# Performance work log

Hardware: AMD Instinct MI355X
Metric: run time of the kernel (lower is better)

Reference implementation:

```python
import jax, jax.numpy as jnp
import numpy as np

D3D, D2D, DTEXT, DPROJ, SEQ_LEN = 256, 768, 3072, 3072, 256
B, S, T = 32, 256, 512


def setup_inputs() -> dict:
    key = jax.random.key(0)
    ks = jax.random.split(key, 9)
    s3 = 1.0 / np.sqrt(D3D)
    s2 = 1.0 / np.sqrt(D2D)
    sf = 1.0 / np.sqrt(DPROJ * 3)
    return {
        "feat_3d": jax.random.normal(ks[0], (B, D3D), jnp.float32),
        "feat_2d": jax.random.normal(ks[1], (B, S, D2D), jnp.float32),
        "feat_text": jax.random.normal(ks[2], (B, T, DTEXT), jnp.float32),
        "W3d": jax.random.uniform(ks[3], (DPROJ, D3D), jnp.float32, -s3, s3),
        "b3d": jax.random.uniform(ks[4], (DPROJ,), jnp.float32, -s3, s3),
        "W2d": jax.random.uniform(ks[5], (DPROJ, D2D), jnp.float32, -s2, s2),
        "b2d": jax.random.uniform(ks[6], (DPROJ,), jnp.float32, -s2, s2),
        "Wf": jax.random.uniform(ks[7], (DPROJ, DPROJ * 3), jnp.float32, -sf, sf),
        "bf": jax.random.uniform(ks[8], (DPROJ,), jnp.float32, -sf, sf),
    }


def reference(feat_3d, feat_2d, feat_text, W3d, b3d, W2d, b2d, Wf, bf):
    # Projections
    f3p = feat_3d @ W3d.T + b3d                      # [B, P]
    f2p = jnp.einsum("bsd,pd->bsp", feat_2d, W2d) + b2d  # [B, S, P]

    # Attention pooling of 2D slice features against global 3D feature
    scores_s = jnp.einsum("bsp,bp->bs", f2p, f3p)    # [B, S]
    w_s = jax.nn.softmax(scores_s, axis=1)
    pooled_2d = jnp.einsum("bs,bsp->bp", w_s, f2p)   # [B, P]

    # Attention pooling of text features against global 3D feature
    scores_t = jnp.einsum("btp,bp->bt", feat_text, f3p)  # [B, T]
    w_t = jax.nn.softmax(scores_t, axis=1)
    pooled_text = jnp.einsum("bt,btp->bp", w_t, feat_text)  # [B, P]

    # All seq_len rows of the original's concatenated input are identical,
    # so compute the fusion GEMM once per batch element and broadcast.
    fused_vec = jnp.concatenate([f3p, pooled_2d, pooled_text], axis=-1) @ Wf.T + bf  # [B, P]
    return jnp.broadcast_to(fused_vec[:, None, :], (fused_vec.shape[0], SEQ_LEN, fused_vec.shape[1]))
```

## Files before the change

### kernel.cpp

```cpp
#include <hip/hip_runtime.h>

#define NB 32
#define NS 256
#define NT 512
#define KD3 256
#define KD2 768
#define NP 3072
#define KFZ 9216

__global__ __launch_bounds__(256) void k1_f3p(const float* __restrict__ f3d,
                                              const float* __restrict__ W3d,
                                              const float* __restrict__ b3d,
                                              float* __restrict__ concatb) {
  int b = blockIdx.x & 31, pc = blockIdx.x >> 5;
  __shared__ float4 xs[KD3 / 4];
  int tid = threadIdx.x;
  if (tid < KD3 / 4) xs[tid] = ((const float4*)(f3d + b * KD3))[tid];
  __syncthreads();
  int p = pc * 256 + tid;
  const float4* wrow = (const float4*)(W3d + (size_t)p * KD3);
  float acc = b3d[p];
#pragma unroll 8
  for (int i = 0; i < KD3 / 4; ++i) {
    float4 w = wrow[i], x = xs[i];
    acc = fmaf(w.x, x.x, acc); acc = fmaf(w.y, x.y, acc);
    acc = fmaf(w.z, x.z, acc); acc = fmaf(w.w, x.w, acc);
  }
  concatb[(size_t)b * KFZ + p] = acc;
}

__global__ __launch_bounds__(256) void k2_gpart(const float* __restrict__ W2d,
                                                const float* __restrict__ concatb,
                                                float* __restrict__ g_part) {
  int dc = blockIdx.x % 3, kc = blockIdx.x / 3;
  __shared__ float xs[NB * 96];
  int tid = threadIdx.x;
  int p0 = kc * 96;
  for (int i = tid; i < NB * 96; i += 256) {
    int bb = i / 96, pp = i - bb * 96;
    xs[i] = concatb[(size_t)bb * KFZ + p0 + pp];
  }
  __syncthreads();
  int d = dc * 256 + tid;
  float acc[NB];
#pragma unroll
  for (int b = 0; b < NB; ++b) acc[b] = 0.f;
  for (int pp = 0; pp < 96; pp += 4) {
    float w0 = W2d[(size_t)(p0 + pp + 0) * KD2 + d];
    float w1 = W2d[(size_t)(p0 + pp + 1) * KD2 + d];
    float w2 = W2d[(size_t)(p0 + pp + 2) * KD2 + d];
    float w3 = W2d[(size_t)(p0 + pp + 3) * KD2 + d];
#pragma unroll
    for (int b = 0; b < NB; ++b) {
      float4 x4 = *(const float4*)&xs[b * 96 + pp];
      acc[b] = fmaf(w0, x4.x, acc[b]); acc[b] = fmaf(w1, x4.y, acc[b]);
      acc[b] = fmaf(w2, x4.z, acc[b]); acc[b] = fmaf(w3, x4.w, acc[b]);
    }
  }
#pragma unroll
  for (int b = 0; b < NB; ++b) g_part[(size_t)(kc * NB + b) * KD2 + d] = acc[b];
}

__global__ __launch_bounds__(256) void k3a_scores(const float* __restrict__ f2d,
                                                  const float* __restrict__ g_part,
                                                  float* __restrict__ w_s) {
  int b = blockIdx.x & 31, sc = blockIdx.x >> 5;
  __shared__ float g[KD2];
  int tid = threadIdx.x;
  for (int i = tid; i < KD2; i += 256) {
    float a = 0.f;
    for (int c = 0; c < 32; ++c) a += g_part[(size_t)(c * NB + b) * KD2 + i];
    g[i] = a;
  }
  __syncthreads();
  int wave = tid >> 6, lane = tid & 63;
  for (int i = 0; i < 16; ++i) {
    int s = sc * 64 + wave * 16 + i;
    const float4* row = (const float4*)(f2d + ((size_t)b * NS + s) * KD2);
    float acc = 0.f;
#pragma unroll
    for (int j = 0; j < 3; ++j) {
      float4 v = row[lane + 64 * j];
      float4 gg = *(const float4*)&g[4 * (lane + 64 * j)];
      acc = fmaf(v.x, gg.x, acc); acc = fmaf(v.y, gg.y, acc);
      acc = fmaf(v.z, gg.z, acc); acc = fmaf(v.w, gg.w, acc);
    }
#pragma unroll
    for (int o = 32; o; o >>= 1) acc += __shfl_xor(acc, o, 64);
    if (lane == 0) w_s[b * NS + s] = acc;
  }
}

template <int N>
__global__ __launch_bounds__(N) void k_softmax(float* __restrict__ w) {
  int b = blockIdx.x, tid = threadIdx.x;
  __shared__ float sm[N / 64];
  __shared__ float stat[2];
  float v = w[(size_t)b * N + tid];
  int wave = tid >> 6, lane = tid & 63;
  float m = v;
#pragma unroll
  for (int o = 32; o; o >>= 1) m = fmaxf(m, __shfl_xor(m, o, 64));
  if (lane == 0) sm[wave] = m;
  __syncthreads();
  if (tid == 0) {
    float mm = sm[0];
    for (int i = 1; i < N / 64; ++i) mm = fmaxf(mm, sm[i]);
    stat[0] = mm;
  }
  __syncthreads();
  float e = __expf(v - stat[0]);
  float s = e;
#pragma unroll
  for (int o = 32; o; o >>= 1) s += __shfl_xor(s, o, 64);
  __syncthreads();
  if (lane == 0) sm[wave] = s;
  __syncthreads();
  if (tid == 0) {
    float ss = 0.f;
    for (int i = 0; i < N / 64; ++i) ss += sm[i];
    stat[1] = ss;
  }
  __syncthreads();
  w[(size_t)b * N + tid] = e / stat[1];
}

__global__ __launch_bounds__(256) void k3c_pool2f(const float* __restrict__ f2d,
                                                  const float* __restrict__ w_s,
                                                  float* __restrict__ p2f) {
  int b = blockIdx.x / 3, dc = blockIdx.x % 3;
  __shared__ float w[NS];
  int tid = threadIdx.x;
  w[tid] = w_s[b * NS + tid];
  __syncthreads();
  int d = dc * 256 + tid;
  float acc = 0.f;
  for (int s = 0; s < NS; ++s)
    acc = fmaf(w[s], f2d[((size_t)b * NS + s) * KD2 + d], acc);
  p2f[b * KD2 + d] = acc;
}

__global__ __launch_bounds__(256) void k4a_scorest(const float* __restrict__ ftx,
                                                   const float* __restrict__ concatb,
                                                   float* __restrict__ w_t) {
  int b = blockIdx.x & 31, tc = blockIdx.x >> 5;
  __shared__ float4 f3[NP / 4];
  int tid = threadIdx.x;
  for (int i = tid; i < NP / 4; i += 256)
    f3[i] = ((const float4*)(concatb + (size_t)b * KFZ))[i];
  __syncthreads();
  int wave = tid >> 6, lane = tid & 63;
  for (int i = 0; i < 16; ++i) {
    int t = tc * 64 + wave * 16 + i;
    const float4* row = (const float4*)(ftx + ((size_t)b * NT + t) * NP);
    float acc = 0.f;
#pragma unroll
    for (int j = 0; j < 12; ++j) {
      float4 v = row[lane + 64 * j];
      float4 gg = f3[lane + 64 * j];
      acc = fmaf(v.x, gg.x, acc); acc = fmaf(v.y, gg.y, acc);
      acc = fmaf(v.z, gg.z, acc); acc = fmaf(v.w, gg.w, acc);
    }
#pragma unroll
    for (int o = 32; o; o >>= 1) acc += __shfl_xor(acc, o, 64);
    if (lane == 0) w_t[b * NT + t] = acc;
  }
}

__global__ __launch_bounds__(256) void k4c_poolt(const float* __restrict__ ftx,
                                                 const float* __restrict__ w_t,
                                                 float* __restrict__ ptp) {
  int b = blockIdx.x & 31;
  int r = blockIdx.x >> 5;
  int pc = r % 3, tc = r / 3;
  __shared__ float w[128];
  int tid = threadIdx.x;
  if (tid < 128) w[tid] = w_t[b * NT + tc * 128 + tid];
  __syncthreads();
  int p4 = pc * 1024 + 4 * tid;
  float4 acc = {0.f, 0.f, 0.f, 0.f};
  const float* base = ftx + ((size_t)b * NT + tc * 128) * NP + p4;
  for (int tt = 0; tt < 128; ++tt) {
    float4 v = *(const float4*)(base + (size_t)tt * NP);
    float ww = w[tt];
    acc.x = fmaf(ww, v.x, acc.x); acc.y = fmaf(ww, v.y, acc.y);
    acc.z = fmaf(ww, v.z, acc.z); acc.w = fmaf(ww, v.w, acc.w);
  }
  *(float4*)(ptp + (size_t)(tc * NB + b) * NP + p4) = acc;
}

__global__ __launch_bounds__(256) void k4d_red(const float* __restrict__ ptp,
                                               float* __restrict__ concatb) {
  int b = blockIdx.x & 31, pc = blockIdx.x >> 5;
  int p = pc * 256 + threadIdx.x;
  float a = 0.f;
#pragma unroll
  for (int c = 0; c < 4; ++c) a += ptp[(size_t)(c * NB + b) * NP + p];
  concatb[(size_t)b * KFZ + 2 * NP + p] = a;
}

__global__ __launch_bounds__(256) void k5_pool2d(const float* __restrict__ W2d,
                                                 const float* __restrict__ b2d,
                                                 const float* __restrict__ p2f,
                                                 float* __restrict__ concatb) {
  int bh = blockIdx.x & 1, pb = blockIdx.x >> 1;
  __shared__ float xs[16 * KD2];
  int tid = threadIdx.x;
  for (int i = tid; i < 16 * KD2; i += 256) xs[i] = p2f[(size_t)(bh * 16) * KD2 + i];
  __syncthreads();
  int wave = tid >> 6, lane = tid & 63;
  for (int pi = 0; pi < 4; ++pi) {
    int p = pb * 16 + wave * 4 + pi;
    const float4* row = (const float4*)(W2d + (size_t)p * KD2);
    float4 wv0 = row[lane], wv1 = row[lane + 64], wv2 = row[lane + 128];
    for (int bb = 0; bb < 16; ++bb) {
      const float* xb = &xs[bb * KD2];
      float4 x0 = *(const float4*)&xb[4 * lane];
      float4 x1 = *(const float4*)&xb[4 * (lane + 64)];
      float4 x2 = *(const float4*)&xb[4 * (lane + 128)];
      float acc = 0.f;
      acc = fmaf(wv0.x, x0.x, acc); acc = fmaf(wv0.y, x0.y, acc);
      acc = fmaf(wv0.z, x0.z, acc); acc = fmaf(wv0.w, x0.w, acc);
      acc = fmaf(wv1.x, x1.x, acc); acc = fmaf(wv1.y, x1.y, acc);
      acc = fmaf(wv1.z, x1.z, acc); acc = fmaf(wv1.w, x1.w, acc);
      acc = fmaf(wv2.x, x2.x, acc); acc = fmaf(wv2.y, x2.y, acc);
      acc = fmaf(wv2.z, x2.z, acc); acc = fmaf(wv2.w, x2.w, acc);
#pragma unroll
      for (int o = 32; o; o >>= 1) acc += __shfl_xor(acc, o, 64);
      if (lane == 0)
        concatb[(size_t)(bh * 16 + bb) * KFZ + NP + p] = acc + b2d[p];
    }
  }
}

__global__ __launch_bounds__(256) void k6_fused(const float* __restrict__ Wf,
                                                const float* __restrict__ concatb,
                                                float* __restrict__ fpart) {
  int kc = blockIdx.x & 15, pb = blockIdx.x >> 4;
  __shared__ float wt[128 * 68];
  __shared__ float xt[32 * 68];
  int tid = threadIdx.x;
  int tp = tid & 31, tb = tid >> 5;
  float acc[4][4];
#pragma unroll
  for (int i = 0; i < 4; ++i)
#pragma unroll
    for (int j = 0; j < 4; ++j) acc[i][j] = 0.f;
  int kbase = kc * 576;
  for (int kt = 0; kt < 9; ++kt) {
    int k0 = kbase + kt * 64;
#pragma unroll
    for (int it = 0; it < 8; ++it) {
      int i = tid + it * 256;
      int row = i >> 4, c4 = (i & 15) * 4;
      *(float4*)&wt[row * 68 + c4] =
          *(const float4*)&Wf[(size_t)(pb * 128 + row) * KFZ + k0 + c4];
    }
#pragma unroll
    for (int it = 0; it < 2; ++it) {
      int i = tid + it * 256;
      int row = i >> 4, c4 = (i & 15) * 4;
      *(float4*)&xt[row * 68 + c4] =
          *(const float4*)&concatb[(size_t)row * KFZ + k0 + c4];
    }
    __syncthreads();
#pragma unroll 4
    for (int kk = 0; kk < 64; kk += 4) {
      float4 wv[4], xv[4];
#pragma unroll
      for (int i = 0; i < 4; ++i) wv[i] = *(const float4*)&wt[(tp + 32 * i) * 68 + kk];
#pragma unroll
      for (int j = 0; j < 4; ++j) xv[j] = *(const float4*)&xt[(tb + 8 * j) * 68 + kk];
#pragma unroll
      for (int i = 0; i < 4; ++i)
#pragma unroll
        for (int j = 0; j < 4; ++j) {
          acc[i][j] = fmaf(wv[i].x, xv[j].x, acc[i][j]);
          acc[i][j] = fmaf(wv[i].y, xv[j].y, acc[i][j]);
          acc[i][j] = fmaf(wv[i].z, xv[j].z, acc[i][j]);
          acc[i][j] = fmaf(wv[i].w, xv[j].w, acc[i][j]);
        }
    }
    __syncthreads();
  }
#pragma unroll
  for (int i = 0; i < 4; ++i)
#pragma unroll
    for (int j = 0; j < 4; ++j)
      fpart[(size_t)(kc * NB + tb + 8 * j) * NP + pb * 128 + tp + 32 * i] = acc[i][j];
}

__global__ __launch_bounds__(256) void k7_bcast(const float* __restrict__ fpart,
                                                const float* __restrict__ bfv,
                                                float* __restrict__ out) {
  int b = blockIdx.x & 31;
  int r = blockIdx.x >> 5;
  int pc = r % 3, sc = r / 3;
  int tid = threadIdx.x;
  int p4 = pc * 1024 + 4 * tid;
  float4 v = *(const float4*)&bfv[p4];
#pragma unroll
  for (int c = 0; c < 16; ++c) {
    float4 a = *(const float4*)&fpart[(size_t)(c * NB + b) * NP + p4];
    v.x += a.x; v.y += a.y; v.z += a.z; v.w += a.w;
  }
  float* obase = out + (size_t)b * NS * NP + p4;
  for (int ss = 0; ss < 64; ++ss) {
    int s = sc * 64 + ss;
    *(float4*)(obase + (size_t)s * NP) = v;
  }
}

extern "C" void kernel_launch(void* const* d_in, const int* in_sizes, int n_in,
                              void* d_out, int out_size, void* d_ws, size_t ws_size,
                              hipStream_t stream) {
  const float* f3d = (const float*)d_in[0];
  const float* f2d = (const float*)d_in[1];
  const float* ftx = (const float*)d_in[2];
  const float* W3d = (const float*)d_in[3];
  const float* b3d = (const float*)d_in[4];
  const float* W2d = (const float*)d_in[5];
  const float* b2d = (const float*)d_in[6];
  const float* Wf  = (const float*)d_in[7];
  const float* bfv = (const float*)d_in[8];
  float* out = (float*)d_out;
  float* ws = (float*)d_ws;

  float* concatb = ws;
  float* g_part  = ws + 294912;
  float* w_s     = ws + 1081344;
  float* p2f     = ws + 1089536;
  float* w_t     = ws + 1114112;
  float* ptp     = ws + 1130496;
  float* fpart   = ws + 1523712;

  k1_f3p<<<384, 256, 0, stream>>>(f3d, W3d, b3d, concatb);
  k2_gpart<<<96, 256, 0, stream>>>(W2d, concatb, g_part);
  k3a_scores<<<128, 256, 0, stream>>>(f2d, g_part, w_s);
  k_softmax<256><<<32, 256, 0, stream>>>(w_s);
  k3c_pool2f<<<96, 256, 0, stream>>>(f2d, w_s, p2f);
  k4a_scorest<<<256, 256, 0, stream>>>(ftx, concatb, w_t);
  k_softmax<512><<<32, 512, 0, stream>>>(w_t);
  k4c_poolt<<<384, 256, 0, stream>>>(ftx, w_t, ptp);
  k4d_red<<<384, 256, 0, stream>>>(ptp, concatb);
  k5_pool2d<<<384, 256, 0, stream>>>(W2d, b2d, p2f, concatb);
  k6_fused<<<384, 256, 0, stream>>>(Wf, concatb, fpart);
  k7_bcast<<<384, 256, 0, stream>>>(fpart, bfv, out);
}
```

Before: 613.8 us.

## Restructure pipeline with online-softmax text pooling and merged multi-role kernels

Text scoring, softmax and pooling are fused into a single pass over feat_text using an online (flash-style) softmax. Per-chunk max/sum partials are merged in a later kernel, so the 200MB text tensor is read once instead of twice. Independent work (the W2d-based score GEMV and the text pass, then the 2D scores and the text reduction) is co-scheduled in the same launches, and the 2D softmax is folded into pooling. The pooled-2D projection becomes a split-K tiled GEMM writing to four partial concat buffers, and the fusion GEMM's tiles are enlarged. This cuts the kernel count from twelve to seven, at the cost of extra partial-buffer traffic and higher register pressure.

```diff
diff --git a/kernel.cpp b/kernel.cpp
--- a/kernel.cpp
+++ b/kernel.cpp
@@ -8,10 +8,22 @@
 #define NP 3072
 #define KFZ 9216
 
+__device__ __forceinline__ float wave_red_sum(float v) {
+#pragma unroll
+  for (int o = 32; o; o >>= 1) v += __shfl_xor(v, o, 64);
+  return v;
+}
+__device__ __forceinline__ float wave_red_max(float v) {
+#pragma unroll
+  for (int o = 32; o; o >>= 1) v = fmaxf(v, __shfl_xor(v, o, 64));
+  return v;
+}
+
 __global__ __launch_bounds__(256) void k1_f3p(const float* __restrict__ f3d,
                                               const float* __restrict__ W3d,
                                               const float* __restrict__ b3d,
-                                              float* __restrict__ concatb) {
+                                              float* __restrict__ c0, float* __restrict__ c1,
+                                              float* __restrict__ c2, float* __restrict__ c3) {
   int b = blockIdx.x & 31, pc = blockIdx.x >> 5;
   __shared__ float4 xs[KD3 / 4];
   int tid = threadIdx.x;
@@ -26,253 +38,226 @@
     acc = fmaf(w.x, x.x, acc); acc = fmaf(w.y, x.y, acc);
     acc = fmaf(w.z, x.z, acc); acc = fmaf(w.w, x.w, acc);
   }
-  concatb[(size_t)b * KFZ + p] = acc;
-}
-
-__global__ __launch_bounds__(256) void k2_gpart(const float* __restrict__ W2d,
-                                                const float* __restrict__ concatb,
-                                                float* __restrict__ g_part) {
-  int dc = blockIdx.x % 3, kc = blockIdx.x / 3;
-  __shared__ float xs[NB * 96];
-  int tid = threadIdx.x;
-  int p0 = kc * 96;
-  for (int i = tid; i < NB * 96; i += 256) {
-    int bb = i / 96, pp = i - bb * 96;
-    xs[i] = concatb[(size_t)bb * KFZ + p0 + pp];
-  }
+  size_t o = (size_t)b * KFZ + p;
+  c0[o] = acc; c1[o] = 0.f; c2[o] = 0.f; c3[o] = 0.f;
+}
+
+__global__ __launch_bounds__(256) void k_L2(const float* __restrict__ ftx,
+                                            const float* __restrict__ W2d,
+                                            const float* __restrict__ c0,
+                                            float* __restrict__ g_part,
+                                            float* __restrict__ Pt,
+                                            float* __restrict__ ml) {
+  __shared__ float4 smem4[768];
+  float* sm = (float*)smem4;
+  int tid = threadIdx.x;
+  if (blockIdx.x < 512) {
+    int b = blockIdx.x & 31, tch = blockIdx.x >> 5;
+    for (int i = tid; i < NP / 4; i += 256)
+      smem4[i] = ((const float4*)(c0 + (size_t)b * KFZ))[i];
+    __syncthreads();
+    int wave = tid >> 6, lane = tid & 63;
+    int t0 = tch * 32 + wave * 8;
+    float m = -3.0e38f, l = 0.f;
+    float4 acc[12];
+#pragma unroll
+    for (int j = 0; j < 12; ++j) acc[j] = make_float4(0.f, 0.f, 0.f, 0.f);
+    for (int r = 0; r < 8; ++r) {
+      const float4* row = (const float4*)(ftx + ((size_t)(b * NT + t0 + r)) * NP);
+      float4 xr[12];
+#pragma unroll
+      for (int j = 0; j < 12; ++j) xr[j] = row[lane + 64 * j];
+      float s = 0.f;
+#pragma unroll
+      for (int j = 0; j < 12; ++j) {
+        float4 f = smem4[lane + 64 * j];
+        s = fmaf(xr[j].x, f.x, s); s = fmaf(xr[j].y, f.y, s);
+        s = fmaf(xr[j].z, f.z, s); s = fmaf(xr[j].w, f.w, s);
+      }
+      s = wave_red_sum(s);
+      float mn = fmaxf(m, s);
+      float al = __expf(m - mn);
+      float e = __expf(s - mn);
+      l = fmaf(l, al, e);
+#pragma unroll
+      for (int j = 0; j < 12; ++j) {
+        acc[j].x = fmaf(acc[j].x, al, e * xr[j].x);
+        acc[j].y = fmaf(acc[j].y, al, e * xr[j].y);
+        acc[j].z = fmaf(acc[j].z, al, e * xr[j].z);
+        acc[j].w = fmaf(acc[j].w, al, e * xr[j].w);
+      }
+      m = mn;
+    }
+    int c = tch * 4 + wave;
+    float4* Pr = (float4*)(Pt + (size_t)(c * NB + b) * NP);
+#pragma unroll
+    for (int j = 0; j < 12; ++j) Pr[lane + 64 * j] = acc[j];
+    if (lane == 0) { ml[(c * NB + b) * 2] = m; ml[(c * NB + b) * 2 + 1] = l; }
+  } else {
+    int id = blockIdx.x - 512;
+    int dc = id % 3, kc = id / 3;
+    int p0 = kc * 96;
+    for (int i = tid; i < NB * 96; i += 256) {
+      int bb = i / 96, pp = i - bb * 96;
+      sm[i] = c0[(size_t)bb * KFZ + p0 + pp];
+    }
+    __syncthreads();
+    int d = dc * 256 + tid;
+    float acc[NB];
+#pragma unroll
+    for (int b = 0; b < NB; ++b) acc[b] = 0.f;
+    for (int pp = 0; pp < 96; pp += 4) {
+      float w0 = W2d[(size_t)(p0 + pp + 0) * KD2 + d];
+      float w1 = W2d[(size_t)(p0 + pp + 1) * KD2 + d];
+      float w2 = W2d[(size_t)(p0 + pp + 2) * KD2 + d];
+      float w3 = W2d[(size_t)(p0 + pp + 3) * KD2 + d];
+#pragma unroll
+      for (int b = 0; b < NB; ++b) {
+        float4 x4 = *(const float4*)&sm[b * 96 + pp];
+        acc[b] = fmaf(w0, x4.x, acc[b]); acc[b] = fmaf(w1, x4.y, acc[b]);
+        acc[b] = fmaf(w2, x4.z, acc[b]); acc[b] = fmaf(w3, x4.w, acc[b]);
+      }
+    }
+#pragma unroll
+    for (int b = 0; b < NB; ++b) g_part[(size_t)(kc * NB + b) * KD2 + d] = acc[b];
+  }
+}
+
+__global__ __launch_bounds__(256) void k_L3(const float* __restrict__ f2d,
+                                            const float* __restrict__ g_part,
+                                            float* __restrict__ sraw,
+                                            const float* __restrict__ Pt,
+                                            const float* __restrict__ ml,
+                                            float* __restrict__ c0, float* __restrict__ c1,
+                                            float* __restrict__ c2, float* __restrict__ c3) {
+  __shared__ float4 sh4[KD2 / 4];
+  float* sh = (float*)sh4;
+  int tid = threadIdx.x;
+  if (blockIdx.x < 128) {
+    int b = blockIdx.x & 31, sc = blockIdx.x >> 5;
+    for (int i = tid; i < KD2; i += 256) {
+      float a = 0.f;
+      for (int c = 0; c < 32; ++c) a += g_part[(size_t)(c * NB + b) * KD2 + i];
+      sh[i] = a;
+    }
+    __syncthreads();
+    int wave = tid >> 6, lane = tid & 63;
+    for (int i = 0; i < 16; ++i) {
+      int s = sc * 64 + wave * 16 + i;
+      const float4* row = (const float4*)(f2d + ((size_t)b * NS + s) * KD2);
+      float acc = 0.f;
+#pragma unroll
+      for (int j = 0; j < 3; ++j) {
+        float4 v = row[lane + 64 * j];
+        float4 g = sh4[lane + 64 * j];
+        acc = fmaf(v.x, g.x, acc); acc = fmaf(v.y, g.y, acc);
+        acc = fmaf(v.z, g.z, acc); acc = fmaf(v.w, g.w, acc);
+      }
+      acc = wave_red_sum(acc);
+      if (lane == 0) sraw[b * NS + s] = acc;
+    }
+  } else {
+    int id = blockIdx.x - 128;
+    int b = id & 31, pc = id >> 5;
+    if (tid < 64) {
+      sh[2 * tid] = ml[(tid * NB + b) * 2];
+      sh[2 * tid + 1] = ml[(tid * NB + b) * 2 + 1];
+    }
+    __syncthreads();
+    float M = -3.0e38f;
+    for (int c = 0; c < 64; ++c) M = fmaxf(M, sh[2 * c]);
+    float denom = 0.f;
+    for (int c = 0; c < 64; ++c) denom += __expf(sh[2 * c] - M) * sh[2 * c + 1];
+    float inv = 1.f / denom;
+    int p4 = pc * 1024 + tid * 4;
+    float4 a = make_float4(0.f, 0.f, 0.f, 0.f);
+    for (int c = 0; c < 64; ++c) {
+      float w = __expf(sh[2 * c] - M);
+      float4 v = *(const float4*)&Pt[(size_t)(c * NB + b) * NP + p4];
+      a.x = fmaf(w, v.x, a.x); a.y = fmaf(w, v.y, a.y);
+      a.z = fmaf(w, v.z, a.z); a.w = fmaf(w, v.w, a.w);
+    }
+    a.x *= inv; a.y *= inv; a.z *= inv; a.w *= inv;
+    size_t o = (size_t)b * KFZ + 2 * NP + p4;
+    float4 z = make_float4(0.f, 0.f, 0.f, 0.f);
+    *(float4*)&c0[o] = a;
+    *(float4*)&c1[o] = z; *(float4*)&c2[o] = z; *(float4*)&c3[o] = z;
+  }
+}
+
+__global__ __launch_bounds__(256) void k3c_sm(const float* __restrict__ f2d,
+                                              const float* __restrict__ sraw,
+                                              float* __restrict__ p2f) {
+  int b = blockIdx.x & 31;
+  int r = blockIdx.x >> 5;
+  int dc = r % 3, sc = r / 3;
+  __shared__ float pr[NS];
+  __shared__ float red[8];
+  int tid = threadIdx.x;
+  int wave = tid >> 6, lane = tid & 63;
+  float v = sraw[b * NS + tid];
+  float mx = wave_red_max(v);
+  if (lane == 0) red[wave] = mx;
   __syncthreads();
-  int d = dc * 256 + tid;
-  float acc[NB];
-#pragma unroll
-  for (int b = 0; b < NB; ++b) acc[b] = 0.f;
-  for (int pp = 0; pp < 96; pp += 4) {
-    float w0 = W2d[(size_t)(p0 + pp + 0) * KD2 + d];
-    float w1 = W2d[(size_t)(p0 + pp + 1) * KD2 + d];
-    float w2 = W2d[(size_t)(p0 + pp + 2) * KD2 + d];
-    float w3 = W2d[(size_t)(p0 + pp + 3) * KD2 + d];
-#pragma unroll
-    for (int b = 0; b < NB; ++b) {
-      float4 x4 = *(const float4*)&xs[b * 96 + pp];
-      acc[b] = fmaf(w0, x4.x, acc[b]); acc[b] = fmaf(w1, x4.y, acc[b]);
-      acc[b] = fmaf(w2, x4.z, acc[b]); acc[b] = fmaf(w3, x4.w, acc[b]);
-    }
-  }
-#pragma unroll
-  for (int b = 0; b < NB; ++b) g_part[(size_t)(kc * NB + b) * KD2 + d] = acc[b];
-}
-
-__global__ __launch_bounds__(256) void k3a_scores(const float* __restrict__ f2d,
-                                                  const float* __restrict__ g_part,
-                                                  float* __restrict__ w_s) {
-  int b = blockIdx.x & 31, sc = blockIdx.x >> 5;
-  __shared__ float g[KD2];
-  int tid = threadIdx.x;
-  for (int i = tid; i < KD2; i += 256) {
-    float a = 0.f;
-    for (int c = 0; c < 32; ++c) a += g_part[(size_t)(c * NB + b) * KD2 + i];
-    g[i] = a;
-  }
+  float M = fmaxf(fmaxf(red[0], red[1]), fmaxf(red[2], red[3]));
+  float e = __expf(v - M);
+  pr[tid] = e;
+  float smv = wave_red_sum(e);
+  if (lane == 0) red[4 + wave] = smv;
   __syncthreads();
-  int wave = tid >> 6, lane = tid & 63;
-  for (int i = 0; i < 16; ++i) {
-    int s = sc * 64 + wave * 16 + i;
-    const float4* row = (const float4*)(f2d + ((size_t)b * NS + s) * KD2);
-    float acc = 0.f;
-#pragma unroll
-    for (int j = 0; j < 3; ++j) {
-      float4 v = row[lane + 64 * j];
-      float4 gg = *(const float4*)&g[4 * (lane + 64 * j)];
-      acc = fmaf(v.x, gg.x, acc); acc = fmaf(v.y, gg.y, acc);
-      acc = fmaf(v.z, gg.z, acc); acc = fmaf(v.w, gg.w, acc);
-    }
-#pragma unroll
-    for (int o = 32; o; o >>= 1) acc += __shfl_xor(acc, o, 64);
-    if (lane == 0) w_s[b * NS + s] = acc;
-  }
-}
-
-template <int N>
-__global__ __launch_bounds__(N) void k_softmax(float* __restrict__ w) {
-  int b = blockIdx.x, tid = threadIdx.x;
-  __shared__ float sm[N / 64];
-  __shared__ float stat[2];
-  float v = w[(size_t)b * N + tid];
-  int wave = tid >> 6, lane = tid & 63;
-  float m = v;
-#pragma unroll
-  for (int o = 32; o; o >>= 1) m = fmaxf(m, __shfl_xor(m, o, 64));
-  if (lane == 0) sm[wave] = m;
-  __syncthreads();
-  if (tid == 0) {
-    float mm = sm[0];
-    for (int i = 1; i < N / 64; ++i) mm = fmaxf(mm, sm[i]);
-    stat[0] = mm;
-  }
-  __syncthreads();
-  float e = __expf(v - stat[0]);
-  float s = e;
-#pragma unroll
-  for (int o = 32; o; o >>= 1) s += __shfl_xor(s, o, 64);
-  __syncthreads();
-  if (lane == 0) sm[wave] = s;
-  __syncthreads();
-  if (tid == 0) {
-    float ss = 0.f;
-    for (int i = 0; i < N / 64; ++i) ss += sm[i];
-    stat[1] = ss;
-  }
-  __syncthreads();
-  w[(size_t)b * N + tid] = e / stat[1];
-}
-
-__global__ __launch_bounds__(256) void k3c_pool2f(const float* __restrict__ f2d,
-                                                  const float* __restrict__ w_s,
-                                                  float* __restrict__ p2f) {
-  int b = blockIdx.x / 3, dc = blockIdx.x % 3;
-  __shared__ float w[NS];
-  int tid = threadIdx.x;
-  w[tid] = w_s[b * NS + tid];
-  __syncthreads();
+  float inv = 1.f / (red[4] + red[5] + red[6] + red[7]);
   int d = dc * 256 + tid;
   float acc = 0.f;
-  for (int s = 0; s < NS; ++s)
-    acc = fmaf(w[s], f2d[((size_t)b * NS + s) * KD2 + d], acc);
-  p2f[b * KD2 + d] = acc;
-}
-
-__global__ __launch_bounds__(256) void k4a_scorest(const float* __restrict__ ftx,
-                                                   const float* __restrict__ concatb,
-                                                   float* __restrict__ w_t) {
-  int b = blockIdx.x & 31, tc = blockIdx.x >> 5;
-  __shared__ float4 f3[NP / 4];
-  int tid = threadIdx.x;
-  for (int i = tid; i < NP / 4; i += 256)
-    f3[i] = ((const float4*)(concatb + (size_t)b * KFZ))[i];
-  __syncthreads();
-  int wave = tid >> 6, lane = tid & 63;
-  for (int i = 0; i < 16; ++i) {
-    int t = tc * 64 + wave * 16 + i;
-    const float4* row = (const float4*)(ftx + ((size_t)b * NT + t) * NP);
-    float acc = 0.f;
-#pragma unroll
-    for (int j = 0; j < 12; ++j) {
-      float4 v = row[lane + 64 * j];
-      float4 gg = f3[lane + 64 * j];
-      acc = fmaf(v.x, gg.x, acc); acc = fmaf(v.y, gg.y, acc);
-      acc = fmaf(v.z, gg.z, acc); acc = fmaf(v.w, gg.w, acc);
-    }
-#pragma unroll
-    for (int o = 32; o; o >>= 1) acc += __shfl_xor(acc, o, 64);
-    if (lane == 0) w_t[b * NT + t] = acc;
-  }
-}
-
-__global__ __launch_bounds__(256) void k4c_poolt(const float* __restrict__ ftx,
-                                                 const float* __restrict__ w_t,
-                                                 float* __restrict__ ptp) {
-  int b = blockIdx.x & 31;
-  int r = blockIdx.x >> 5;
-  int pc = r % 3, tc = r / 3;
-  __shared__ float w[128];
-  int tid = threadIdx.x;
-  if (tid < 128) w[tid] = w_t[b * NT + tc * 128 + tid];
-  __syncthreads();
-  int p4 = pc * 1024 + 4 * tid;
-  float4 acc = {0.f, 0.f, 0.f, 0.f};
-  const float* base = ftx + ((size_t)b * NT + tc * 128) * NP + p4;
-  for (int tt = 0; tt < 128; ++tt) {
-    float4 v = *(const float4*)(base + (size_t)tt * NP);
-    float ww = w[tt];
-    acc.x = fmaf(ww, v.x, acc.x); acc.y = fmaf(ww, v.y, acc.y);
-    acc.z = fmaf(ww, v.z, acc.z); acc.w = fmaf(ww, v.w, acc.w);
-  }
-  *(float4*)(ptp + (size_t)(tc * NB + b) * NP + p4) = acc;
-}
-
-__global__ __launch_bounds__(256) void k4d_red(const float* __restrict__ ptp,
-                                               float* __restrict__ concatb) {
-  int b = blockIdx.x & 31, pc = blockIdx.x >> 5;
-  int p = pc * 256 + threadIdx.x;
-  float a = 0.f;
-#pragma unroll
-  for (int c = 0; c < 4; ++c) a += ptp[(size_t)(c * NB + b) * NP + p];
-  concatb[(size_t)b * KFZ + 2 * NP + p] = a;
+  const float* base = f2d + ((size_t)b * NS + sc * 128) * KD2 + d;
+#pragma unroll 8
+  for (int s = 0; s < 128; ++s)
+    acc = fmaf(pr[sc * 128 + s], base[(size_t)s * KD2], acc);
+  p2f[(size_t)(sc * NB + b) * KD2 + d] = acc * inv;
 }
 
 __global__ __launch_bounds__(256) void k5_pool2d(const float* __restrict__ W2d,
                                                  const float* __restrict__ b2d,
                                                  const float* __restrict__ p2f,
-                                                 float* __restrict__ concatb) {
-  int bh = blockIdx.x & 1, pb = blockIdx.x >> 1;
-  __shared__ float xs[16 * KD2];
-  int tid = threadIdx.x;
-  for (int i = tid; i < 16 * KD2; i += 256) xs[i] = p2f[(size_t)(bh * 16) * KD2 + i];
-  __syncthreads();
-  int wave = tid >> 6, lane = tid & 63;
-  for (int pi = 0; pi < 4; ++pi) {
-    int p = pb * 16 + wave * 4 + pi;
-    const float4* row = (const float4*)(W2d + (size_t)p * KD2);
-    float4 wv0 = row[lane], wv1 = row[lane + 64], wv2 = row[lane + 128];
-    for (int bb = 0; bb < 16; ++bb) {
-      const float* xb = &xs[bb * KD2];
-      float4 x0 = *(const float4*)&xb[4 * lane];
-      float4 x1 = *(const float4*)&xb[4 * (lane + 64)];
-      float4 x2 = *(const float4*)&xb[4 * (lane + 128)];
-      float acc = 0.f;
-      acc = fmaf(wv0.x, x0.x, acc); acc = fmaf(wv0.y, x0.y, acc);
-      acc = fmaf(wv0.z, x0.z, acc); acc = fmaf(wv0.w, x0.w, acc);
-      acc = fmaf(wv1.x, x1.x, acc); acc = fmaf(wv1.y, x1.y, acc);
-      acc = fmaf(wv1.z, x1.z, acc); acc = fmaf(wv1.w, x1.w, acc);
-      acc = fmaf(wv2.x, x2.x, acc); acc = fmaf(wv2.y, x2.y, acc);
-      acc = fmaf(wv2.z, x2.z, acc); acc = fmaf(wv2.w, x2.w, acc);
-#pragma unroll
-      for (int o = 32; o; o >>= 1) acc += __shfl_xor(acc, o, 64);
-      if (lane == 0)
-        concatb[(size_t)(bh * 16 + bb) * KFZ + NP + p] = acc + b2d[p];
-    }
-  }
-}
-
-__global__ __launch_bounds__(256) void k6_fused(const float* __restrict__ Wf,
-                                                const float* __restrict__ concatb,
-                                                float* __restrict__ fpart) {
-  int kc = blockIdx.x & 15, pb = blockIdx.x >> 4;
-  __shared__ float wt[128 * 68];
-  __shared__ float xt[32 * 68];
+                                                 float* __restrict__ c0, float* __restrict__ c1,
+                                                 float* __restrict__ c2, float* __restrict__ c3) {
+  int pb = blockIdx.x >> 2, ks = blockIdx.x & 3;
+  __shared__ __align__(16) float wt[64 * 68];
+  __shared__ __align__(16) float xt[32 * 68];
   int tid = threadIdx.x;
   int tp = tid & 31, tb = tid >> 5;
-  float acc[4][4];
-#pragma unroll
-  for (int i = 0; i < 4; ++i)
+  float acc[2][4];
+#pragma unroll
+  for (int i = 0; i < 2; ++i)
 #pragma unroll
     for (int j = 0; j < 4; ++j) acc[i][j] = 0.f;
-  int kbase = kc * 576;
-  for (int kt = 0; kt < 9; ++kt) {
-    int k0 = kbase + kt * 64;
-#pragma unroll
-    for (int it = 0; it < 8; ++it) {
-      int i = tid + it * 256;
-      int row = i >> 4, c4 = (i & 15) * 4;
+  for (int dk = 0; dk < 3; ++dk) {
+    int d0 = ks * 192 + dk * 64;
+#pragma unroll
+    for (int it = 0; it < 4; ++it) {
+      int idx = tid + it * 256;
+      int row = idx >> 4, c4 = (idx & 15) * 4;
       *(float4*)&wt[row * 68 + c4] =
-          *(const float4*)&Wf[(size_t)(pb * 128 + row) * KFZ + k0 + c4];
+          *(const float4*)&W2d[(size_t)(pb * 64 + row) * KD2 + d0 + c4];
     }
 #pragma unroll
     for (int it = 0; it < 2; ++it) {
-      int i = tid + it * 256;
-      int row = i >> 4, c4 = (i & 15) * 4;
-      *(float4*)&xt[row * 68 + c4] =
-          *(const float4*)&concatb[(size_t)row * KFZ + k0 + c4];
+      int idx = tid + it * 256;
+      int row = idx >> 4, c4 = (idx & 15) * 4;
+      float4 a = *(const float4*)&p2f[(size_t)row * KD2 + d0 + c4];
+      float4 bq = *(const float4*)&p2f[(size_t)(NB + row) * KD2 + d0 + c4];
+      a.x += bq.x; a.y += bq.y; a.z += bq.z; a.w += bq.w;
+      *(float4*)&xt[row * 68 + c4] = a;
     }
     __syncthreads();
 #pragma unroll 4
     for (int kk = 0; kk < 64; kk += 4) {
-      float4 wv[4], xv[4];
-#pragma unroll
-      for (int i = 0; i < 4; ++i) wv[i] = *(const float4*)&wt[(tp + 32 * i) * 68 + kk];
+      float4 wv[2], xv[4];
+#pragma unroll
+      for (int i = 0; i < 2; ++i) wv[i] = *(const float4*)&wt[(tp + 32 * i) * 68 + kk];
 #pragma unroll
       for (int j = 0; j < 4; ++j) xv[j] = *(const float4*)&xt[(tb + 8 * j) * 68 + kk];
 #pragma unroll
-      for (int i = 0; i < 4; ++i)
+      for (int i = 0; i < 2; ++i)
 #pragma unroll
         for (int j = 0; j < 4; ++j) {
           acc[i][j] = fmaf(wv[i].x, xv[j].x, acc[i][j]);
@@ -283,11 +268,80 @@
     }
     __syncthreads();
   }
-#pragma unroll
-  for (int i = 0; i < 4; ++i)
+  float* dst = (ks == 0) ? c0 : (ks == 1) ? c1 : (ks == 2) ? c2 : c3;
+#pragma unroll
+  for (int i = 0; i < 2; ++i) {
+    int p = pb * 64 + tp + 32 * i;
+    float bias = (ks == 0) ? b2d[p] : 0.f;
 #pragma unroll
     for (int j = 0; j < 4; ++j)
-      fpart[(size_t)(kc * NB + tb + 8 * j) * NP + pb * 128 + tp + 32 * i] = acc[i][j];
+      dst[(size_t)(tb + 8 * j) * KFZ + NP + p] = acc[i][j] + bias;
+  }
+}
+
+__global__ __launch_bounds__(256) void k6_fused(const float* __restrict__ Wf,
+                                                const float* __restrict__ c0,
+                                                const float* __restrict__ c1,
+                                                const float* __restrict__ c2,
+                                                const float* __restrict__ c3,
+                                                float* __restrict__ fpart) {
+  int pb = blockIdx.x >> 4, kc = blockIdx.x & 15;
+  __shared__ __align__(16) float wt[192 * 68];
+  __shared__ __align__(16) float xt[32 * 68];
+  int tid = threadIdx.x;
+  int tp = tid & 31, tb = tid >> 5;
+  float acc[6][4];
+#pragma unroll
+  for (int i = 0; i < 6; ++i)
+#pragma unroll
+    for (int j = 0; j < 4; ++j) acc[i][j] = 0.f;
+  for (int kt = 0; kt < 9; ++kt) {
+    int k0 = kc * 576 + kt * 64;
+#pragma unroll
+    for (int it = 0; it < 12; ++it) {
+      int idx = tid + it * 256;
+      int row = idx >> 4, c4 = (idx & 15) * 4;
+      *(float4*)&wt[row * 68 + c4] =
+          *(const float4*)&Wf[(size_t)(pb * 192 + row) * KFZ + k0 + c4];
+    }
+#pragma unroll
+    for (int it = 0; it < 2; ++it) {
+      int idx = tid + it * 256;
+      int row = idx >> 4, c4 = (idx & 15) * 4;
+      size_t o = (size_t)row * KFZ + k0 + c4;
+      float4 a = *(const float4*)&c0[o];
+      float4 v1 = *(const float4*)&c1[o];
+      float4 v2 = *(const float4*)&c2[o];
+      float4 v3 = *(const float4*)&c3[o];
+      a.x += v1.x + v2.x + v3.x; a.y += v1.y + v2.y + v3.y;
+      a.z += v1.z + v2.z + v3.z; a.w += v1.w + v2.w + v3.w;
+      *(float4*)&xt[row * 68 + c4] = a;
+    }
+    __syncthreads();
+#pragma unroll 4
+    for (int kk = 0; kk < 64; kk += 4) {
+      float4 wv[6], xv[4];
+#pragma unroll
+      for (int i = 0; i < 6; ++i) wv[i] = *(const float4*)&wt[(tp + 32 * i) * 68 + kk];
+#pragma unroll
+      for (int j = 0; j < 4; ++j) xv[j] = *(const float4*)&xt[(tb + 8 * j) * 68 + kk];
+#pragma unroll
+      for (int i = 0; i < 6; ++i)
+#pragma unroll
+        for (int j = 0; j < 4; ++j) {
+          acc[i][j] = fmaf(wv[i].x, xv[j].x, acc[i][j]);
+          acc[i][j] = fmaf(wv[i].y, xv[j].y, acc[i][j]);
+          acc[i][j] = fmaf(wv[i].z, xv[j].z, acc[i][j]);
+          acc[i][j] = fmaf(wv[i].w, xv[j].w, acc[i][j]);
+        }
+    }
+    __syncthreads();
+  }
+#pragma unroll
+  for (int i = 0; i < 6; ++i)
+#pragma unroll
+    for (int j = 0; j < 4; ++j)
+      fpart[(size_t)(kc * NB + tb + 8 * j) * NP + pb * 192 + tp + 32 * i] = acc[i][j];
 }
 
 __global__ __launch_bounds__(256) void k7_bcast(const float* __restrict__ fpart,
@@ -326,24 +380,22 @@
   float* out = (float*)d_out;
   float* ws = (float*)d_ws;
 
-  float* concatb = ws;
-  float* g_part  = ws + 294912;
-  float* w_s     = ws + 1081344;
-  float* p2f     = ws + 1089536;
-  float* w_t     = ws + 1114112;
-  float* ptp     = ws + 1130496;
-  float* fpart   = ws + 1523712;
-
-  k1_f3p<<<384, 256, 0, stream>>>(f3d, W3d, b3d, concatb);
-  k2_gpart<<<96, 256, 0, stream>>>(W2d, concatb, g_part);
-  k3a_scores<<<128, 256, 0, stream>>>(f2d, g_part, w_s);
-  k_softmax<256><<<32, 256, 0, stream>>>(w_s);
-  k3c_pool2f<<<96, 256, 0, stream>>>(f2d, w_s, p2f);
-  k4a_scorest<<<256, 256, 0, stream>>>(ftx, concatb, w_t);
-  k_softmax<512><<<32, 512, 0, stream>>>(w_t);
-  k4c_poolt<<<384, 256, 0, stream>>>(ftx, w_t, ptp);
-  k4d_red<<<384, 256, 0, stream>>>(ptp, concatb);
-  k5_pool2d<<<384, 256, 0, stream>>>(W2d, b2d, p2f, concatb);
-  k6_fused<<<384, 256, 0, stream>>>(Wf, concatb, fpart);
+  float* c0     = ws;
+  float* c1     = ws + 294912;
+  float* c2     = ws + 589824;
+  float* c3     = ws + 884736;
+  float* g_part = ws + 1179648;
+  float* sraw   = ws + 1966080;
+  float* p2f    = ws + 1974272;
+  float* ml     = ws + 2023424;
+  float* Pt     = ws + 2027520;
+  float* fpart  = ws + 8318976;
+
+  k1_f3p<<<384, 256, 0, stream>>>(f3d, W3d, b3d, c0, c1, c2, c3);
+  k_L2<<<608, 256, 0, stream>>>(ftx, W2d, c0, g_part, Pt, ml);
+  k_L3<<<224, 256, 0, stream>>>(f2d, g_part, sraw, Pt, ml, c0, c1, c2, c3);
+  k3c_sm<<<192, 256, 0, stream>>>(f2d, sraw, p2f);
+  k5_pool2d<<<192, 256, 0, stream>>>(W2d, b2d, p2f, c0, c1, c2, c3);
+  k6_fused<<<256, 256, 0, stream>>>(Wf, c0, c1, c2, c3, fpart);
   k7_bcast<<<384, 256, 0, stream>>>(fpart, bfv, out);
 }
```

Result: faster. 553.1 us (-9.9%).
